# Performance work log

Hardware: AMD Instinct MI355X
Metric: run time of the kernel (lower is better)

Reference implementation:

```python
import jax, jax.numpy as jnp
import numpy as np

NEG_SLOPE = 0.01  # torch F.leaky_relu default


def _leaky_relu(v):
    return jnp.where(v >= 0, v, NEG_SLOPE * v)


def _att_layer(t, w1, w2):
    # t: [b, c, n] ; SE-style channel attention with scalar gate
    y = t.mean(axis=-1)                                   # [b, c] (AdaptiveAvgPool1d(1))
    y = jax.nn.sigmoid(jax.nn.relu(y @ w1.T) @ w2.T)       # [b, 1]
    return t * y[:, :, None]


def _avwgcn(x, node_emb, supports, cheb, wpool, bpool, iw, ib, gw, gb,
            a1w1, a1w2, a2w1, a2w2):
    # x: [b, n, c_in]; supports/cheb: [k, n, n]
    b, n, _ = x.shape
    weights = jnp.einsum('nd,dkio->nkio', node_emb, wpool)   # per-node dyn weights
    bias = node_emb @ bpool                                  # [n, o]
    x_g = jnp.einsum('knm,bmc->bnkc', supports, x)           # [b, n, k, c_in]
    x_gconv0 = jnp.einsum('bnki,nkio->bno', x_g, weights) + bias
    x0 = x @ iw.T + ib                                       # init_gconv: [b, n, o]
    x_g1 = jnp.einsum('knm,bmc->bnkc', cheb, x0).reshape(b, n, -1)
    x_gconv1 = x_g1 @ gw.T + gb                              # [b, n, o]
    out = (_att_layer(_leaky_relu(x_gconv0).transpose(0, 2, 1), a1w1, a1w2)
           + _att_layer(_leaky_relu(x_gconv1).transpose(0, 2, 1), a2w1, a2w2))
    return out.transpose(0, 2, 1)                            # [b, n, o]


def _cheb_supports(L, k):
    n = L.shape[0]
    s = [jnp.eye(n, dtype=L.dtype), L]
    for _ in range(2, k):
        s.append(2.0 * L @ s[-1] - s[-2])
    return jnp.stack(s, axis=0)  # [k, n, n]


B, N, DIN, DOUT, K, ED = 64, 1024, 32, 64, 3, 16
CIN = DIN + DOUT  # 96 (gate/update input = cat(x, state))


def setup_inputs() -> dict:
    key = jax.random.key(0)
    ks = jax.random.split(key, 32)
    g = lambda i, shape, s=0.1: jax.random.normal(ks[i], shape, dtype=jnp.float32) * s
    inp = {
        'x': jax.random.normal(ks[0], (B, N, DIN), dtype=jnp.float32),
        'state': jax.random.normal(ks[1], (B, N, DOUT), dtype=jnp.float32),
        'node_embeddings': jax.random.normal(ks[2], (N, ED), dtype=jnp.float32),
        'learned_tilde': jax.random.normal(ks[3], (N, N), dtype=jnp.float32) / np.sqrt(N),
        'cheb_polynomials': jax.random.normal(ks[4], (K, N, N), dtype=jnp.float32) / np.sqrt(N),
        # gate AVWGCN: dim_in=96, dim_out=2*DOUT=128
        'gate_wpool': g(5, (ED, K, CIN, 2 * DOUT)),
        'gate_bpool': g(6, (ED, 2 * DOUT)),
        'gate_iw': g(7, (2 * DOUT, CIN)), 'gate_ib': g(8, (2 * DOUT,)),
        'gate_gw': g(9, (2 * DOUT, 2 * DOUT * K)), 'gate_gb': g(10, (2 * DOUT,)),
        'gate_a1w1': g(11, (2 * DOUT // 16, 2 * DOUT)), 'gate_a1w2': g(12, (1, 2 * DOUT // 16)),
        'gate_a2w1': g(13, (2 * DOUT // 16, 2 * DOUT)), 'gate_a2w2': g(14, (1, 2 * DOUT // 16)),
        # update AVWGCN: dim_in=96, dim_out=DOUT=64
        'upd_wpool': g(15, (ED, K, CIN, DOUT)),
        'upd_bpool': g(16, (ED, DOUT)),
        'upd_iw': g(17, (DOUT, CIN)), 'upd_ib': g(18, (DOUT,)),
        'upd_gw': g(19, (DOUT, DOUT * K)), 'upd_gb': g(20, (DOUT,)),
        'upd_a1w1': g(21, (DOUT // 16, DOUT)), 'upd_a1w2': g(22, (1, DOUT // 16)),
        'upd_a2w1': g(23, (DOUT // 16, DOUT)), 'upd_a2w2': g(24, (1, DOUT // 16)),
    }
    return inp


def reference(x, state, node_embeddings, learned_tilde, cheb_polynomials,
              gate_wpool, gate_bpool, gate_iw, gate_ib, gate_gw, gate_gb,
              gate_a1w1, gate_a1w2, gate_a2w1, gate_a2w2,
              upd_wpool, upd_bpool, upd_iw, upd_ib, upd_gw, upd_gb,
              upd_a1w1, upd_a1w2, upd_a2w1, upd_a2w2):
    supports = _cheb_supports(learned_tilde, K)  # [k, n, n]
    inp_state = jnp.concatenate([x, state], axis=-1)  # [b, n, din+dout]
    z_r = jax.nn.sigmoid(_avwgcn(inp_state, node_embeddings, supports, cheb_polynomials,
                                 gate_wpool, gate_bpool, gate_iw, gate_ib, gate_gw, gate_gb,
                                 gate_a1w1, gate_a1w2, gate_a2w1, gate_a2w2))
    z, r = jnp.split(z_r, 2, axis=-1)
    candidate = jnp.concatenate([x, z * state], axis=-1)
    hc = jnp.tanh(_avwgcn(candidate, node_embeddings, supports, cheb_polynomials,
                          upd_wpool, upd_bpool, upd_iw, upd_ib, upd_gw, upd_gb,
                          upd_a1w1, upd_a1w2, upd_a2w1, upd_a2w2))
    h = r * state + (1.0 - r) * hc
    return h
```

## Files before the change

### kernel.cpp

```cpp
#include <hip/hip_runtime.h>
#include <hip/hip_bf16.h>
#include <math.h>


#define B_  64
#define N_  1024
#define CIN_ 96
#define R_  288

typedef __attribute__((ext_vector_type(8))) short bf16x8;
typedef __attribute__((ext_vector_type(4))) float f32x4;
typedef unsigned short u16;
typedef unsigned int u32;

__device__ __forceinline__ float lrelu(float v) { return v >= 0.f ? v : 0.01f * v; }
__device__ __forceinline__ float sigmoidf_(float u) { return 1.f / (1.f + expf(-u)); }
__device__ __forceinline__ u16 f2b(float f) {
  union { float f; u32 u; } c; c.f = f;
  u32 u = c.u;
  return (u16)((u + 0x7FFFu + ((u >> 16) & 1u)) >> 16);
}
__device__ __forceinline__ float b2f(u16 u) {
  union { u32 x; float f; } c; c.x = ((u32)u) << 16; return c.f;
}
__device__ __forceinline__ void gload_lds16(const u16* gp, u16* lp) {
  __builtin_amdgcn_global_load_lds((const __attribute__((address_space(1))) u32*)gp,
                                   (__attribute__((address_space(3))) u32*)lp, 16, 0, 0);
}

__global__ __launch_bounds__(256) void concat_bf2(const float* __restrict__ x,
                                                  const float* __restrict__ st,
                                                  float* __restrict__ inp,
                                                  u16* __restrict__ inpb) {
  size_t t = (size_t)blockIdx.x * 256 + threadIdx.x;
  if (t >= (size_t)B_ * N_ * CIN_) return;
  int i = (int)(t % CIN_);
  size_t v = t / CIN_;
  size_t b = v & 63, n = v >> 6;
  float f = (i < 32) ? x[(b * N_ + n) * 32 + i] : st[(b * N_ + n) * 64 + (i - 32)];
  inp[t] = f;
  inpb[t] = f2b(f);
}

__global__ __launch_bounds__(256) void conv_f2b(const float* __restrict__ in,
                                                u16* __restrict__ out, int n4) {
  int t = blockIdx.x * 256 + threadIdx.x;
  if (t >= n4) return;
  float4 v = ((const float4*)in)[t];
  ushort4 o;
  o.x = f2b(v.x); o.y = f2b(v.y); o.z = f2b(v.z); o.w = f2b(v.w);
  ((ushort4*)out)[t] = o;
}

__global__ __launch_bounds__(256) void split_hilo(const float* __restrict__ in,
                                                  u16* __restrict__ hi,
                                                  u16* __restrict__ lo, int n4) {
  int t = blockIdx.x * 256 + threadIdx.x;
  if (t >= n4) return;
  float4 v = ((const float4*)in)[t];
  ushort4 h, l;
  h.x = f2b(v.x); l.x = f2b(v.x - b2f(h.x));
  h.y = f2b(v.y); l.y = f2b(v.y - b2f(h.y));
  h.z = f2b(v.z); l.z = f2b(v.z - b2f(h.z));
  h.w = f2b(v.w); l.w = f2b(v.w - b2f(h.w));
  ((ushort4*)hi)[t] = h;
  ((ushort4*)lo)[t] = l;
}

__global__ __launch_bounds__(256) void transpose_split(const float* __restrict__ in,
                                                       u16* __restrict__ hiT,
                                                       u16* __restrict__ loT) {
  __shared__ float t[32][33];
  const int tid = threadIdx.x;
  const int j0 = blockIdx.x * 32, r0 = blockIdx.y * 32;
  const int tc = tid & 31, tr = tid >> 5;
#pragma unroll
  for (int q = 0; q < 4; ++q)
    t[tr + q * 8][tc] = in[(size_t)(r0 + tr + q * 8) * 1024 + j0 + tc];
  __syncthreads();
  const int jj = tid >> 3, rq = (tid & 7) * 4;
  ushort4 h, l;
#pragma unroll
  for (int q = 0; q < 4; ++q) {
    float v = t[rq + q][jj];
    u16 hh = f2b(v);
    ((u16*)&h)[q] = hh;
    ((u16*)&l)[q] = f2b(v - b2f(hh));
  }
  *(ushort4*)(hiT + (size_t)(j0 + jj) * N_ + r0 + rq) = h;
  *(ushort4*)(loT + (size_t)(j0 + jj) * N_ + r0 + rq) = l;
}

__global__ __launch_bounds__(256) void transpose_b2b(const u16* __restrict__ Z, int Zs,
                                                     int Ctot, u16* __restrict__ Zt) {
  __shared__ u16 t[32][36];
  const int tid = threadIdx.x;
  const int c0 = blockIdx.x * 32, n0 = blockIdx.y * 32, b = blockIdx.z;
  {
    const int i = tid >> 3, c4 = (tid & 7) * 4;
    ushort4 v = *(const ushort4*)(Z + ((size_t)(n0 + i) * 64 + b) * Zs + c0 + c4);
    t[i][c4] = v.x; t[i][c4 + 1] = v.y; t[i][c4 + 2] = v.z; t[i][c4 + 3] = v.w;
  }
  __syncthreads();
  {
    const int c = tid >> 3, n4 = (tid & 7) * 4;
    ushort4 o;
    o.x = t[n4][c]; o.y = t[n4 + 1][c]; o.z = t[n4 + 2][c]; o.w = t[n4 + 3][c];
    *(ushort4*)(Zt + (size_t)(b * Ctot + c0 + c) * 1024 + n0 + n4) = o;
  }
}

__global__ __launch_bounds__(256) void mfma_l2p(const u16* __restrict__ Lhi,
                                                const u16* __restrict__ Llo,
                                                const u16* __restrict__ LhiT,
                                                const u16* __restrict__ LloT,
                                                float* __restrict__ P) {
  __shared__ u16 Asl[64 * 64];
  __shared__ u16 Bsl[64 * 64];
  const int tid = threadIdx.x;
  const int w = tid >> 6, lane = tid & 63;
  const int m0 = blockIdx.y * 64, n0 = blockIdx.x * 64;
  const int ph = blockIdx.z;
  const int wr = w >> 1, wc = w & 1;
  const int sr = lane >> 3, so = lane & 7;
  const int cl = lane & 15, q4 = lane >> 4;
  f32x4 acc[2][2] = {};

  const u16* A = (ph == 1) ? Llo : Lhi;
  const u16* B = (ph == 2) ? LloT : LhiT;
  for (int k0 = 0; k0 < 1024; k0 += 64) {
    __syncthreads();
#pragma unroll
    for (int i = 0; i < 2; ++i) {
      const int r = i * 32 + w * 8 + sr;
      const int o = so ^ (r & 7);
      gload_lds16(A + (size_t)(m0 + r) * 1024 + k0 + o * 8, Asl + (i * 32 + w * 8) * 64);
      gload_lds16(B + (size_t)(n0 + r) * 1024 + k0 + o * 8, Bsl + (i * 32 + w * 8) * 64);
    }
    __syncthreads();
#pragma unroll
    for (int kk = 0; kk < 2; ++kk) {
      bf16x8 af[2], bfr[2];
#pragma unroll
      for (int mi = 0; mi < 2; ++mi) {
        const int ra = wr * 32 + mi * 16 + cl;
        af[mi] = *(const bf16x8*)(Asl + ra * 64 + ((kk * 4 + q4) ^ (ra & 7)) * 8);
      }
#pragma unroll
      for (int ni = 0; ni < 2; ++ni) {
        const int rb = wc * 32 + ni * 16 + cl;
        bfr[ni] = *(const bf16x8*)(Bsl + rb * 64 + ((kk * 4 + q4) ^ (rb & 7)) * 8);
      }
#pragma unroll
      for (int mi = 0; mi < 2; ++mi)
#pragma unroll
        for (int ni = 0; ni < 2; ++ni)
          acc[mi][ni] = __builtin_amdgcn_mfma_f32_16x16x32_bf16(af[mi], bfr[ni], acc[mi][ni], 0, 0, 0);
    }
  }
  float* Pz = P + ((size_t)ph << 20);
#pragma unroll
  for (int mi = 0; mi < 2; ++mi)
#pragma unroll
    for (int ni = 0; ni < 2; ++ni) {
      const int j = n0 + wc * 32 + ni * 16 + cl;
#pragma unroll
      for (int r = 0; r < 4; ++r) {
        const int m = m0 + wr * 32 + mi * 16 + q4 * 4 + r;
        Pz[(size_t)m * 1024 + j] = acc[mi][ni][r];
      }
    }
}

__global__ __launch_bounds__(256) void l2_finish(const float* __restrict__ P,
                                                 u16* __restrict__ Y) {
  int t = blockIdx.x * 256 + threadIdx.x;
  float4 a = ((const float4*)P)[t];
  float4 b = ((const float4*)(P + 1048576))[t];
  float4 c = ((const float4*)(P + 2097152))[t];
  int e = t << 2;
  int m = e >> 10, j = e & 1023;
  ushort4 o;
  o.x = f2b(2.f * (a.x + b.x + c.x) - (m == j     ? 1.f : 0.f));
  o.y = f2b(2.f * (a.y + b.y + c.y) - (m == j + 1 ? 1.f : 0.f));
  o.z = f2b(2.f * (a.z + b.z + c.z) - (m == j + 2 ? 1.f : 0.f));
  o.w = f2b(2.f * (a.w + b.w + c.w) - (m == j + 3 ? 1.f : 0.f));
  ((ushort4*)Y)[t] = o;
}

__global__ __launch_bounds__(512) void mfma_stack_w(const u16* __restrict__ A,
                                                    const u16* __restrict__ Bt,
                                                    float* __restrict__ Y, int J) {
  __shared__ u16 Asl[2][128 * 64];
  __shared__ u16 Bsl[2][256 * 64];
  const int tid = threadIdx.x;
  const int w = tid >> 6, lane = tid & 63;
  const int m0 = blockIdx.y * 128, n0 = blockIdx.x * 256;
  const int wr = w >> 2, wc = w & 3;
  const int sr = lane >> 3, so = lane & 7;
  const int cl = lane & 15, q4 = lane >> 4;
  f32x4 acc[4][4] = {};

  auto STAGE = [&](u16* Ad, u16* Bd, int k0) {
#pragma unroll
    for (int i = 0; i < 2; ++i) {
      const int r = i * 64 + w * 8 + sr;
      const int o = so ^ (r & 7);
      gload_lds16(A + (size_t)(m0 + r) * 1024 + k0 + o * 8, Ad + (i * 64 + w * 8) * 64);
    }
#pragma unroll
    for (int i = 0; i < 4; ++i) {
      const int r = i * 64 + w * 8 + sr;
      const int o = so ^ (r & 7);
      gload_lds16(Bt + (size_t)(n0 + r) * 1024 + k0 + o * 8, Bd + (i * 64 + w * 8) * 64);
    }
  };
  auto COMPUTE = [&](const u16* As, const u16* Bs) {
#pragma unroll
    for (int kk = 0; kk < 2; ++kk) {
      bf16x8 af[4], bfr[4];
#pragma unroll
      for (int mi = 0; mi < 4; ++mi) {
        const int ra = wr * 64 + mi * 16 + cl;
        af[mi] = *(const bf16x8*)(As + ra * 64 + ((kk * 4 + q4) ^ (ra & 7)) * 8);
      }
#pragma unroll
      for (int ni = 0; ni < 4; ++ni) {
        const int rb = wc * 64 + ni * 16 + cl;
        bfr[ni] = *(const bf16x8*)(Bs + rb * 64 + ((kk * 4 + q4) ^ (rb & 7)) * 8);
      }
#pragma unroll
      for (int mi = 0; mi < 4; ++mi)
#pragma unroll
        for (int ni = 0; ni < 4; ++ni)
          acc[mi][ni] = __builtin_amdgcn_mfma_f32_16x16x32_bf16(af[mi], bfr[ni], acc[mi][ni], 0, 0, 0);
    }
  };

  STAGE(Asl[0], Bsl[0], 0);
  for (int k0 = 0; k0 < 1024; k0 += 128) {
    STAGE(Asl[1], Bsl[1], k0 + 64);
    asm volatile("s_waitcnt vmcnt(6)" ::: "memory");
    __builtin_amdgcn_s_barrier();
    __builtin_amdgcn_sched_barrier(0);
    COMPUTE(Asl[0], Bsl[0]);
    asm volatile("s_waitcnt lgkmcnt(0)" ::: "memory");
    __builtin_amdgcn_s_barrier();
    __builtin_amdgcn_sched_barrier(0);
    if (k0 + 128 < 1024) {
      STAGE(Asl[0], Bsl[0], k0 + 128);
      asm volatile("s_waitcnt vmcnt(6)" ::: "memory");
    } else {
      asm volatile("s_waitcnt vmcnt(0)" ::: "memory");
    }
    __builtin_amdgcn_s_barrier();
    __builtin_amdgcn_sched_barrier(0);
    COMPUTE(Asl[1], Bsl[1]);
    asm volatile("s_waitcnt lgkmcnt(0)" ::: "memory");
    __builtin_amdgcn_s_barrier();
    __builtin_amdgcn_sched_barrier(0);
  }
#pragma unroll
  for (int mi = 0; mi < 4; ++mi)
#pragma unroll
    for (int ni = 0; ni < 4; ++ni) {
      const int j = n0 + wc * 64 + ni * 16 + cl;
#pragma unroll
      for (int r = 0; r < 4; ++r) {
        const int m = m0 + wr * 64 + mi * 16 + q4 * 4 + r;
        Y[(size_t)m * J + j] = acc[mi][ni][r];
      }
    }
}

template <int O, int OSH>
__global__ __launch_bounds__(128) void vgen2(const float* __restrict__ gw,
                                             const float* __restrict__ iw,
                                             const float* __restrict__ ib,
                                             int Ctot,
                                             u16* __restrict__ Vb,
                                             float* __restrict__ ball) {
  const int c = blockIdx.x;
  const int col = threadIdx.x;
  if (c >= Ctot) {
    if (col < 96) Vb[(size_t)c * 96 + col] = 0;
    else if (col == 96) ball[c] = 0.f;
    return;
  }
  __shared__ float sg[O];
  const int o = c & (O - 1), k = c >> OSH;
  const float* g = gw + (size_t)o * (3 * O) + (size_t)k * O;
  for (int e = col; e < O; e += 128) sg[e] = g[e];
  __syncthreads();
  if (col < 96) {
    float s = 0.f;
#pragma unroll
    for (int j = 0; j < O; ++j) s += sg[j] * iw[j * 96 + col];
    Vb[(size_t)c * 96 + col] = f2b(s);
  } else if (col == 96) {
    float s = 0.f;
#pragma unroll
    for (int j = 0; j < O; ++j) s += sg[j] * ib[j];
    ball[c] = s;
  }
}

__global__ __launch_bounds__(256) void zgemm(const u16* __restrict__ A,
                                             const u16* __restrict__ Bt,
                                             const float* __restrict__ ball,
                                             u16* __restrict__ Z, int Zs) {
  __shared__ u16 Asl[128 * 32];
  __shared__ u16 Bsl[128 * 32];
  const int tid = threadIdx.x;
  const int w = tid >> 6, lane = tid & 63;
  const int m0 = blockIdx.y * 128, n0 = blockIdx.x * 128;
  const int wr = w >> 1, wc = w & 1;
  const int sr = lane >> 2, so = lane & 3;
  const int cl = lane & 15, q4 = lane >> 4;
  f32x4 acc[4][4] = {};
  for (int k0 = 0; k0 < 96; k0 += 32) {
    __syncthreads();
#pragma unroll
    for (int i = 0; i < 2; ++i) {
      const int r = i * 64 + w * 16 + sr;
      const int o = so ^ (r & 3);
      gload_lds16(A + (size_t)(m0 + r) * 96 + k0 + o * 8, Asl + (i * 64 + w * 16) * 32);
      gload_lds16(Bt + (size_t)(n0 + r) * 96 + k0 + o * 8, Bsl + (i * 64 + w * 16) * 32);
    }
    __syncthreads();
    bf16x8 af[4], bfr[4];
#pragma unroll
    for (int mi = 0; mi < 4; ++mi) {
      const int ra = wr * 64 + mi * 16 + cl;
      af[mi] = *(const bf16x8*)(Asl + ra * 32 + (q4 ^ (ra & 3)) * 8);
    }
#pragma unroll
    for (int ni = 0; ni < 4; ++ni) {
      const int rb = wc * 64 + ni * 16 + cl;
      bfr[ni] = *(const bf16x8*)(Bsl + rb * 32 + (q4 ^ (rb & 3)) * 8);
    }
#pragma unroll
    for (int mi = 0; mi < 4; ++mi)
#pragma unroll
      for (int ni = 0; ni < 4; ++ni)
        acc[mi][ni] = __builtin_amdgcn_mfma_f32_16x16x32_bf16(af[mi], bfr[ni], acc[mi][ni], 0, 0, 0);
  }
#pragma unroll
  for (int mi = 0; mi < 4; ++mi)
#pragma unroll
    for (int ni = 0; ni < 4; ++ni) {
      const int c = n0 + wc * 64 + ni * 16 + cl;
      const float bb = ball[c];
#pragma unroll
      for (int r = 0; r < 4; ++r) {
        const int m = m0 + wr * 64 + mi * 16 + q4 * 4 + r;
        Z[(size_t)m * Zs + c] = f2b(acc[mi][ni][r] + bb);
      }
    }
}

__global__ __launch_bounds__(512) void mfma_k3(const u16* __restrict__ A3,
                                               const u16* __restrict__ Zt,
                                               const float* __restrict__ gb,
                                               float* __restrict__ Y,
                                               int J, int obits) {
  __shared__ u16 Asl[2][128 * 64];
  __shared__ u16 Bsl[2][128 * 64];
  const int tid = threadIdx.x;
  const int w = tid >> 6, lane = tid & 63;
  const int m0 = blockIdx.y * 128, n0 = blockIdx.x * 128;
  const int wr = w >> 2, wc = w & 3;
  const int sr = lane >> 3, so = lane & 7;
  const int cl = lane & 15, q4 = lane >> 4;
  const int omask = (1 << obits) - 1;
  f32x4 acc[4][2] = {};

  auto STAGE = [&](u16* Ad, u16* Bd, int k0) {
    const int kb = k0 >> 10, ko = k0 & 1023;
#pragma unroll
    for (int i = 0; i < 2; ++i) {
      const int r = i * 64 + w * 8 + sr;
      const int o = so ^ (r & 7);
      gload_lds16(A3 + (size_t)kb * 1048576 + (size_t)(m0 + r) * 1024 + ko + o * 8,
                  Ad + (i * 64 + w * 8) * 64);
      const int jp = n0 + r;
      const int brow = (((jp >> obits) * 3 + kb) << obits) | (jp & omask);
      gload_lds16(Zt + (size_t)brow * 1024 + ko + o * 8, Bd + (i * 64 + w * 8) * 64);
    }
  };
  auto COMPUTE = [&](const u16* As, const u16* Bs) {
#pragma unroll
    for (int kk = 0; kk < 2; ++kk) {
      bf16x8 af[4], bfr[2];
#pragma unroll
      for (int mi = 0; mi < 4; ++mi) {
        const int ra = wr * 64 + mi * 16 + cl;
        af[mi] = *(const bf16x8*)(As + ra * 64 + ((kk * 4 + q4) ^ (ra & 7)) * 8);
      }
#pragma unroll
      for (int ni = 0; ni < 2; ++ni) {
        const int rb = wc * 32 + ni * 16 + cl;
        bfr[ni] = *(const bf16x8*)(Bs + rb * 64 + ((kk * 4 + q4) ^ (rb & 7)) * 8);
      }
#pragma unroll
      for (int mi = 0; mi < 4; ++mi)
#pragma unroll
        for (int ni = 0; ni < 2; ++ni)
          acc[mi][ni] = __builtin_amdgcn_mfma_f32_16x16x32_bf16(af[mi], bfr[ni], acc[mi][ni], 0, 0, 0);
    }
  };

  STAGE(Asl[0], Bsl[0], 0);
  for (int k0 = 0; k0 < 3072; k0 += 128) {
    STAGE(Asl[1], Bsl[1], k0 + 64);
    asm volatile("s_waitcnt vmcnt(4)" ::: "memory");
    __builtin_amdgcn_s_barrier();
    __builtin_amdgcn_sched_barrier(0);
    COMPUTE(Asl[0], Bsl[0]);
    asm volatile("s_waitcnt lgkmcnt(0)" ::: "memory");
    __builtin_amdgcn_s_barrier();
    __builtin_amdgcn_sched_barrier(0);
    if (k0 + 128 < 3072) {
      STAGE(Asl[0], Bsl[0], k0 + 128);
      asm volatile("s_waitcnt vmcnt(4)" ::: "memory");
    } else {
      asm volatile("s_waitcnt vmcnt(0)" ::: "memory");
    }
    __builtin_amdgcn_s_barrier();
    __builtin_amdgcn_sched_barrier(0);
    COMPUTE(Asl[1], Bsl[1]);
    asm volatile("s_waitcnt lgkmcnt(0)" ::: "memory");
    __builtin_amdgcn_s_barrier();
    __builtin_amdgcn_sched_barrier(0);
  }
#pragma unroll
  for (int mi = 0; mi < 4; ++mi)
#pragma unroll
    for (int ni = 0; ni < 2; ++ni) {
      const int j = n0 + wc * 32 + ni * 16 + cl;
      const float bb = gb[j & omask];
#pragma unroll
      for (int r = 0; r < 4; ++r) {
        const int m = m0 + wr * 64 + mi * 16 + q4 * 4 + r;
        Y[(size_t)m * J + j] = acc[mi][ni][r] + bb;
      }
    }
}

__global__ __launch_bounds__(512) void mfma_k3w(const u16* __restrict__ A3,
                                                const u16* __restrict__ Zt,
                                                const float* __restrict__ gb,
                                                float* __restrict__ Y,
                                                int J, int obits) {
  __shared__ u16 Asl[2][128 * 64];
  __shared__ u16 Bsl[2][256 * 64];
  const int tid = threadIdx.x;
  const int w = tid >> 6, lane = tid & 63;
  const int m0 = blockIdx.y * 128, n0 = blockIdx.x * 256;
  const int wr = w >> 2, wc = w & 3;
  const int sr = lane >> 3, so = lane & 7;
  const int cl = lane & 15, q4 = lane >> 4;
  const int omask = (1 << obits) - 1;
  f32x4 acc[4][4] = {};

  auto STAGE = [&](u16* Ad, u16* Bd, int k0) {
    const int kb = k0 >> 10, ko = k0 & 1023;
#pragma unroll
    for (int i = 0; i < 2; ++i) {
      const int r = i * 64 + w * 8 + sr;
      const int o = so ^ (r & 7);
      gload_lds16(A3 + (size_t)kb * 1048576 + (size_t)(m0 + r) * 1024 + ko + o * 8,
                  Ad + (i * 64 + w * 8) * 64);
    }
#pragma unroll
    for (int i = 0; i < 4; ++i) {
      const int r = i * 64 + w * 8 + sr;
      const int o = so ^ (r & 7);
      const int jp = n0 + r;
      const int brow = (((jp >> obits) * 3 + kb) << obits) | (jp & omask);
      gload_lds16(Zt + (size_t)brow * 1024 + ko + o * 8, Bd + (i * 64 + w * 8) * 64);
    }
  };
  auto COMPUTE = [&](const u16* As, const u16* Bs) {
#pragma unroll
    for (int kk = 0; kk < 2; ++kk) {
      bf16x8 af[4], bfr[4];
#pragma unroll
      for (int mi = 0; mi < 4; ++mi) {
        const int ra = wr * 64 + mi * 16 + cl;
        af[mi] = *(const bf16x8*)(As + ra * 64 + ((kk * 4 + q4) ^ (ra & 7)) * 8);
      }
#pragma unroll
      for (int ni = 0; ni < 4; ++ni) {
        const int rb = wc * 64 + ni * 16 + cl;
        bfr[ni] = *(const bf16x8*)(Bs + rb * 64 + ((kk * 4 + q4) ^ (rb & 7)) * 8);
      }
#pragma unroll
      for (int mi = 0; mi < 4; ++mi)
#pragma unroll
        for (int ni = 0; ni < 4; ++ni)
          acc[mi][ni] = __builtin_amdgcn_mfma_f32_16x16x32_bf16(af[mi], bfr[ni], acc[mi][ni], 0, 0, 0);
    }
  };

  STAGE(Asl[0], Bsl[0], 0);
  for (int k0 = 0; k0 < 3072; k0 += 128) {
    STAGE(Asl[1], Bsl[1], k0 + 64);
    asm volatile("s_waitcnt vmcnt(6)" ::: "memory");
    __builtin_amdgcn_s_barrier();
    __builtin_amdgcn_sched_barrier(0);
    COMPUTE(Asl[0], Bsl[0]);
    asm volatile("s_waitcnt lgkmcnt(0)" ::: "memory");
    __builtin_amdgcn_s_barrier();
    __builtin_amdgcn_sched_barrier(0);
    if (k0 + 128 < 3072) {
      STAGE(Asl[0], Bsl[0], k0 + 128);
      asm volatile("s_waitcnt vmcnt(6)" ::: "memory");
    } else {
      asm volatile("s_waitcnt vmcnt(0)" ::: "memory");
    }
    __builtin_amdgcn_s_barrier();
    __builtin_amdgcn_sched_barrier(0);
    COMPUTE(Asl[1], Bsl[1]);
    asm volatile("s_waitcnt lgkmcnt(0)" ::: "memory");
    __builtin_amdgcn_s_barrier();
    __builtin_amdgcn_sched_barrier(0);
  }
#pragma unroll
  for (int mi = 0; mi < 4; ++mi)
#pragma unroll
    for (int ni = 0; ni < 4; ++ni) {
      const int j = n0 + wc * 64 + ni * 16 + cl;
      const float bb = gb[j & omask];
#pragma unroll
      for (int r = 0; r < 4; ++r) {
        const int m = m0 + wr * 64 + mi * 16 + q4 * 4 + r;
        Y[(size_t)m * J + j] = acc[mi][ni][r] + bb;
      }
    }
}

template <int OW>
__global__ __launch_bounds__(256) void weightgen3w(const float* __restrict__ emb,
                                                   const float* __restrict__ wpool,
                                                   u16* __restrict__ W) {
  const int tid = threadIdx.x;
  const int ro = blockIdx.x * 256 + tid;
  const int r = ro / OW, o = ro % OW;
  const int n0 = blockIdx.y * 64;
  __shared__ float semb[64][17];
  for (int e = tid; e < 1024; e += 256) semb[e >> 4][e & 15] = emb[(n0 + (e >> 4)) * 16 + (e & 15)];
  __syncthreads();
  float wv[16];
#pragma unroll
  for (int d = 0; d < 16; ++d) wv[d] = wpool[((size_t)d * R_ + r) * OW + o];
#pragma unroll 4
  for (int n = 0; n < 64; ++n) {
    float s = 0.f;
#pragma unroll
    for (int d = 0; d < 16; ++d) s += semb[n][d] * wv[d];
    W[(size_t)(n0 + n) * (R_ * OW) + ro] = f2b(s);
  }
}

template <int OW>
__global__ __launch_bounds__(256) void pernode9(const float* __restrict__ xa,
                                                const float* __restrict__ xbc,
                                                const u16* __restrict__ W,
                                                const float* __restrict__ emb,
                                                const float* __restrict__ bpool,
                                                float* __restrict__ outp) {
  constexpr int QO = OW / 32;
  const int n = blockIdx.x;
  const int tid = threadIdx.x;
  __shared__ __align__(16) float sW[32][OW + 4];
  __shared__ __align__(16) float sX[32][68];
  __shared__ float semb[16];
  if (tid < 16) semb[tid] = emb[n * 16 + tid];
  const int tx = tid & 31, tb = tid >> 5;
  const int lb = tid >> 2, li = (tid & 3) * 8;
  float acc[8][QO] = {};
  const u16* Wn = W + (size_t)n * (R_ * OW);

  for (int c = 0; c < 9; ++c) {
    const int k = c / 3, i0 = (c % 3) * 32;
    const float* xk = (k == 0) ? (xa + (size_t)n * 6144)
                               : (xbc + ((size_t)(k - 1) * 1024 + n) * 6144);
    __syncthreads();
    {
#pragma unroll
      for (int it = 0; it < OW / 64; ++it) {
        const int slot = it * 256 + tid;
        const int row = slot / (OW / 8), o8 = (slot % (OW / 8)) * 8;
        uint4 v = *(const uint4*)(Wn + (size_t)(c * 32 + row) * OW + o8);
        float4 f0, f1;
        f0.x = b2f((u16)(v.x & 0xFFFF)); f0.y = b2f((u16)(v.x >> 16));
        f0.z = b2f((u16)(v.y & 0xFFFF)); f0.w = b2f((u16)(v.y >> 16));
        f1.x = b2f((u16)(v.z & 0xFFFF)); f1.y = b2f((u16)(v.z >> 16));
        f1.z = b2f((u16)(v.w & 0xFFFF)); f1.w = b2f((u16)(v.w >> 16));
        *(float4*)&sW[row][o8] = f0;
        *(float4*)&sW[row][o8 + 4] = f1;
      }
    }
    {
      const float* p = xk + (size_t)lb * 96 + i0 + li;
      float4 v0 = *(const float4*)p;
      float4 v1 = *(const float4*)(p + 4);
      sX[li + 0][lb] = v0.x; sX[li + 1][lb] = v0.y;
      sX[li + 2][lb] = v0.z; sX[li + 3][lb] = v0.w;
      sX[li + 4][lb] = v1.x; sX[li + 5][lb] = v1.y;
      sX[li + 6][lb] = v1.z; sX[li + 7][lb] = v1.w;
    }
    __syncthreads();
#pragma unroll
    for (int il = 0; il < 32; ++il) {
      float4 xv0 = *(const float4*)&sX[il][tb * 8];
      float4 xv1 = *(const float4*)&sX[il][tb * 8 + 4];
      float xv[8] = {xv0.x, xv0.y, xv0.z, xv0.w, xv1.x, xv1.y, xv1.z, xv1.w};
      float wv[QO];
      if constexpr (QO == 4) {
        float4 w4 = *(const float4*)&sW[il][tx * 4];
        wv[0] = w4.x; wv[1] = w4.y; wv[2] = w4.z; wv[3] = w4.w;
      } else {
        float2 w2 = *(const float2*)&sW[il][tx * 2];
        wv[0] = w2.x; wv[1] = w2.y;
      }
#pragma unroll
      for (int j = 0; j < 8; ++j)
#pragma unroll
        for (int q = 0; q < QO; ++q) acc[j][q] += xv[j] * wv[q];
    }
  }
  float bias[QO];
#pragma unroll
  for (int q = 0; q < QO; ++q) {
    int o = tx * QO + q;
    float s = 0.f;
#pragma unroll
    for (int d = 0; d < 16; ++d) s += semb[d] * bpool[d * OW + o];
    bias[q] = s;
  }
#pragma unroll
  for (int j = 0; j < 8; ++j) {
    size_t base = ((size_t)n * B_ + tb * 8 + j) * OW + tx * QO;
#pragma unroll
    for (int q = 0; q < QO; ++q) outp[base + q] = acc[j][q] + bias[q];
  }
}

template <int C>
__global__ __launch_bounds__(256) void att_reduce(const float* __restrict__ A0,
                                                  const float* __restrict__ A1,
                                                  float* __restrict__ part0,
                                                  float* __restrict__ part1) {
  constexpr int C4 = C / 4;
  constexpr int H = 256 / C4;
  const int chunk = blockIdx.x;
  const int b = blockIdx.y;
  const int tid = threadIdx.x;
  const int c4 = tid % C4, h = tid / C4;
  __shared__ float4 r0[256], r1[256];
  float4 s0 = {0.f, 0.f, 0.f, 0.f}, s1 = {0.f, 0.f, 0.f, 0.f};
  const float4* p0 = (const float4*)(A0 + (size_t)b * C) + c4;
  const float4* p1 = (const float4*)(A1 + (size_t)b * C) + c4;
  const size_t stride = (size_t)B_ * C4;
  for (int n = chunk * 64 + h; n < chunk * 64 + 64; n += H) {
    float4 v0 = p0[(size_t)n * stride];
    float4 v1 = p1[(size_t)n * stride];
    s0.x += lrelu(v0.x); s0.y += lrelu(v0.y); s0.z += lrelu(v0.z); s0.w += lrelu(v0.w);
    s1.x += lrelu(v1.x); s1.y += lrelu(v1.y); s1.z += lrelu(v1.z); s1.w += lrelu(v1.w);
  }
  r0[tid] = s0; r1[tid] = s1;
  __syncthreads();
  if (h == 0) {
    for (int hh = 1; hh < H; ++hh) {
      float4 a = r0[c4 + hh * C4], bb = r1[c4 + hh * C4];
      s0.x += a.x; s0.y += a.y; s0.z += a.z; s0.w += a.w;
      s1.x += bb.x; s1.y += bb.y; s1.z += bb.z; s1.w += bb.w;
    }
    ((float4*)(part0 + ((size_t)b * 16 + chunk) * C))[c4] = s0;
    ((float4*)(part1 + ((size_t)b * 16 + chunk) * C))[c4] = s1;
  }
}

template <int C, int HID>
__global__ __launch_bounds__(256) void att_finish(const float* __restrict__ part0,
                                                  const float* __restrict__ part1,
                                                  const float* __restrict__ w11,
                                                  const float* __restrict__ w12,
                                                  const float* __restrict__ w21,
                                                  const float* __restrict__ w22,
                                                  float* __restrict__ sout) {
  const int b = blockIdx.x;
  const int tid = threadIdx.x;
  __shared__ float sm0[C], sm1[C];
  __shared__ float h0[HID], h1[HID];
  if (tid < C) {
    float s0 = 0.f, s1 = 0.f;
    for (int ch = 0; ch < 16; ++ch) {
      s0 += part0[((size_t)b * 16 + ch) * C + tid];
      s1 += part1[((size_t)b * 16 + ch) * C + tid];
    }
    sm0[tid] = s0 * (1.f / N_); sm1[tid] = s1 * (1.f / N_);
  }
  __syncthreads();
  if (tid < HID) {
    float a = 0.f;
    for (int cc = 0; cc < C; ++cc) a += sm0[cc] * w11[tid * C + cc];
    h0[tid] = fmaxf(a, 0.f);
  } else if (tid >= 32 && tid < 32 + HID) {
    int j = tid - 32;
    float a = 0.f;
    for (int cc = 0; cc < C; ++cc) a += sm1[cc] * w21[j * C + cc];
    h1[j] = fmaxf(a, 0.f);
  }
  __syncthreads();
  if (tid == 0) {
    float a = 0.f;
    for (int j = 0; j < HID; ++j) a += h0[j] * w12[j];
    sout[b] = sigmoidf_(a);
  } else if (tid == 32) {
    float a = 0.f;
    for (int j = 0; j < HID; ++j) a += h1[j] * w22[j];
    sout[B_ + b] = sigmoidf_(a);
  }
}

__global__ __launch_bounds__(256) void gate_combine_b2(const float* __restrict__ a0,
                                                       const float* __restrict__ a1,
                                                       const float* __restrict__ s12,
                                                       const float* __restrict__ x,
                                                       const float* __restrict__ st,
                                                       float* __restrict__ cand,
                                                       u16* __restrict__ candb,
                                                       float* __restrict__ rbuf) {
  size_t t = (size_t)blockIdx.x * 256 + threadIdx.x;
  if (t >= (size_t)B_ * N_ * 64) return;
  int c = (int)(t & 63);
  int b = (int)((t >> 6) & 63);
  int n = (int)(t >> 12);
  float s1 = s12[b], s2 = s12[B_ + b];
  size_t nb = (size_t)n * B_ + b;
  size_t i128 = nb * 128;
  float uz = s1 * lrelu(a0[i128 + c]) + s2 * lrelu(a1[i128 + c]);
  float ur = s1 * lrelu(a0[i128 + 64 + c]) + s2 * lrelu(a1[i128 + 64 + c]);
  float z = sigmoidf_(uz);
  float r = sigmoidf_(ur);
  float stv = st[((size_t)b * N_ + n) * 64 + c];
  float zs = z * stv;
  cand[nb * CIN_ + 32 + c] = zs;
  candb[nb * CIN_ + 32 + c] = f2b(zs);
  rbuf[nb * 64 + c] = r;
  if (c < 32) {
    float xv = x[((size_t)b * N_ + n) * 32 + c];
    cand[nb * CIN_ + c] = xv;
    candb[nb * CIN_ + c] = f2b(xv);
  }
}

__global__ __launch_bounds__(256) void final_h(const float* __restrict__ a0,
                                               const float* __restrict__ a1,
                                               const float* __restrict__ s12,
                                               const float* __restrict__ rbuf,
                                               const float* __restrict__ st,
                                               float* __restrict__ out) {
  size_t t = (size_t)blockIdx.x * 256 + threadIdx.x;
  if (t >= (size_t)B_ * N_ * 64) return;
  int o = (int)(t & 63);
  int n = (int)((t >> 6) & 1023);
  int b = (int)(t >> 16);
  float s1 = s12[b], s2 = s12[B_ + b];
  size_t nb = ((size_t)n * B_ + b) * 64 + o;
  float u = s1 * lrelu(a0[nb]) + s2 * lrelu(a1[nb]);
  float hc = tanhf(u);
  float r = rbuf[nb];
  out[t] = r * st[t] + (1.f - r) * hc;
}

extern "C" void kernel_launch(void* const* d_in, const int* in_sizes, int n_in,
                              void* d_out, int out_size, void* d_ws, size_t ws_size,
                              hipStream_t stream) {
  const float* x       = (const float*)d_in[0];
  const float* state   = (const float*)d_in[1];
  const float* emb     = (const float*)d_in[2];
  const float* Ltil    = (const float*)d_in[3];
  const float* cheb    = (const float*)d_in[4];
  const float* g_wpool = (const float*)d_in[5];
  const float* g_bpool = (const float*)d_in[6];
  const float* g_iw    = (const float*)d_in[7];
  const float* g_ib    = (const float*)d_in[8];
  const float* g_gw    = (const float*)d_in[9];
  const float* g_gb    = (const float*)d_in[10];
  const float* g_a1w1  = (const float*)d_in[11];
  const float* g_a1w2  = (const float*)d_in[12];
  const float* g_a2w1  = (const float*)d_in[13];
  const float* g_a2w2  = (const float*)d_in[14];
  const float* u_wpool = (const float*)d_in[15];
  const float* u_bpool = (const float*)d_in[16];
  const float* u_iw    = (const float*)d_in[17];
  const float* u_ib    = (const float*)d_in[18];
  const float* u_gw    = (const float*)d_in[19];
  const float* u_gb    = (const float*)d_in[20];
  const float* u_a1w1  = (const float*)d_in[21];
  const float* u_a1w2  = (const float*)d_in[22];
  const float* u_a2w1  = (const float*)d_in[23];
  const float* u_a2w2  = (const float*)d_in[24];
  float* out = (float*)d_out;

  float* ws    = (float*)d_ws;
  float* inp   = ws;
  u16*   inpb  = (u16*)(ws + 6291456);
  float* t12   = ws + 9437184;
  u16*   Zbuf  = (u16*)t12;
  u16*   Wbuf  = (u16*)(ws + 22020096);
  u16*   Wbuf128 = Wbuf;
  u16*   Btp   = (u16*)(ws + 31457280);
  u16*   Zt    = Wbuf;
  float* acc1  = ws + 34603008;
  float* acc0  = ws + 42991616;
  u16*   LbStk = (u16*)(ws + 51380224);
  u16*   chebb = (u16*)(ws + 52428800);
  float* s12   = ws + 54001664;
  float* s12u  = ws + 54001792;
  float* part0 = ws + 54001920;
  float* part1 = ws + 54132992;
  float* rbuf  = ws + 54264064;
  u16*   Vbg   = (u16*)(ws + 58458368);
  float* bag   = ws + 58476800;
  u16*   Vbu   = (u16*)(ws + 58477184);
  float* bau   = ws + 58489472;
  u16*   LhiT  = (u16*)(ws + 58489728);
  u16*   LloT  = (u16*)(ws + 59014016);
  u16*   Llo   = (u16*)(ws + 59538304);

  dim3 blk(256);
  dim3 blk512(512);

  split_hilo<<<1024, blk, 0, stream>>>(Ltil, LbStk, Llo, 262144);
  transpose_split<<<dim3(32, 32), blk, 0, stream>>>(Ltil, LhiT, LloT);
  mfma_l2p<<<dim3(16, 16, 3), blk, 0, stream>>>(LbStk, Llo, LhiT, LloT, t12);
  l2_finish<<<1024, blk, 0, stream>>>(t12, LbStk + 1048576);
  conv_f2b<<<3072, blk, 0, stream>>>(cheb, chebb, 786432);

  concat_bf2<<<24576, blk, 0, stream>>>(x, state, inp, inpb);
  transpose_b2b<<<dim3(3, 32, 64), blk, 0, stream>>>(inpb, 96, 96, Btp);
  mfma_stack_w<<<dim3(24, 16), blk512, 0, stream>>>(LbStk, Btp, t12, 6144);
  vgen2<128, 7><<<384, dim3(128), 0, stream>>>(g_gw, g_iw, g_ib, 384, Vbg, bag);
  weightgen3w<128><<<dim3(144, 16), blk, 0, stream>>>(emb, g_wpool, Wbuf128);
  pernode9<128><<<1024, blk, 0, stream>>>(inp, t12, Wbuf128, emb, g_bpool, acc0);
  zgemm<<<dim3(3, 512), blk, 0, stream>>>(inpb, Vbg, bag, Zbuf, 384);
  transpose_b2b<<<dim3(12, 32, 64), blk, 0, stream>>>(Zbuf, 384, 384, Zt);
  mfma_k3w<<<dim3(32, 8), blk512, 0, stream>>>(chebb, Zt, g_gb, acc1, 8192, 7);
  att_reduce<128><<<dim3(16, 64), blk, 0, stream>>>(acc0, acc1, part0, part1);
  att_finish<128, 8><<<64, blk, 0, stream>>>(part0, part1, g_a1w1, g_a1w2, g_a2w1, g_a2w2, s12);
  gate_combine_b2<<<16384, blk, 0, stream>>>(acc0, acc1, s12, x, state, inp, inpb, rbuf);

  transpose_b2b<<<dim3(3, 32, 64), blk, 0, stream>>>(inpb, 96, 96, Btp);
  mfma_stack_w<<<dim3(24, 16), blk512, 0, stream>>>(LbStk, Btp, t12, 6144);
  vgen2<64, 6><<<256, dim3(128), 0, stream>>>(u_gw, u_iw, u_ib, 192, Vbu, bau);
  weightgen3w<64><<<dim3(72, 16), blk, 0, stream>>>(emb, u_wpool, Wbuf);
  pernode9<64><<<1024, blk, 0, stream>>>(inp, t12, Wbuf, emb, u_bpool, acc0);
  zgemm<<<dim3(2, 512), blk, 0, stream>>>(inpb, Vbu, bau, Zbuf, 256);
  transpose_b2b<<<dim3(6, 32, 64), blk, 0, stream>>>(Zbuf, 256, 192, Zt);
  mfma_k3<<<dim3(32, 8), blk512, 0, stream>>>(chebb, Zt, u_gb, acc1, 4096, 6);
  att_reduce<64><<<dim3(16, 64), blk, 0, stream>>>(acc0, acc1, part0, part1);
  att_finish<64, 4><<<64, blk, 0, stream>>>(part0, part1, u_a1w1, u_a1w2, u_a2w1, u_a2w2, s12u);
  final_h<<<16384, blk, 0, stream>>>(acc0, acc1, s12u, rbuf, state, out);
}
```

Before: 695.8 us.

## Move per-node dynamic-weight GEMM to bf16 MFMA with hi/lo split inputs

Rewrites the per-node graph-conv kernel so it uses bf16 MFMA 16x16x32 instructions instead of scalar fp32 FMAs. Activations are split into bf16 hi and lo parts to keep accuracy, which doubles the MFMA count. To feed the A operand, wpool is now transposed up front and the generated per-node weights are stored output-major. Weights go global-to-LDS directly with XOR swizzles, which removes the bf16-to-fp32 unpack in shared memory. The cost is two extra small transpose launches and the reuse of workspace regions that earlier kernels had already consumed.

Result: faster. 631.2 us (-9.3%).

```diff
diff --git a/kernel.cpp b/kernel.cpp
--- a/kernel.cpp
+++ b/kernel.cpp
@@ -108,6 +108,22 @@
     o.x = t[n4][c]; o.y = t[n4 + 1][c]; o.z = t[n4 + 2][c]; o.w = t[n4 + 3][c];
     *(ushort4*)(Zt + (size_t)(b * Ctot + c0 + c) * 1024 + n0 + n4) = o;
   }
+}
+
+__global__ __launch_bounds__(256) void wpool_tr(const float* __restrict__ wp,
+                                                float* __restrict__ wpT, int OW) {
+  __shared__ float t[32][33];
+  const int tid = threadIdx.x;
+  const int r0 = blockIdx.x * 32, o0 = blockIdx.y * 32, d = blockIdx.z;
+  const size_t base = (size_t)d * 288 * OW;
+  const int c = tid & 31, q0 = tid >> 5;
+#pragma unroll
+  for (int q = 0; q < 4; ++q)
+    t[q0 + q * 8][c] = wp[base + (size_t)(r0 + q0 + q * 8) * OW + o0 + c];
+  __syncthreads();
+#pragma unroll
+  for (int q = 0; q < 4; ++q)
+    wpT[base + (size_t)(o0 + q0 + q * 8) * 288 + r0 + c] = t[c][q0 + q * 8];
 }
 
 __global__ __launch_bounds__(256) void mfma_l2p(const u16* __restrict__ Lhi,
@@ -540,112 +556,125 @@
     }
 }
 
-template <int OW>
-__global__ __launch_bounds__(256) void weightgen3w(const float* __restrict__ emb,
-                                                   const float* __restrict__ wpool,
-                                                   u16* __restrict__ W) {
+template <int SZ>
+__global__ __launch_bounds__(256) void weightgen5(const float* __restrict__ emb,
+                                                  const float* __restrict__ wpT,
+                                                  u16* __restrict__ W) {
   const int tid = threadIdx.x;
   const int ro = blockIdx.x * 256 + tid;
-  const int r = ro / OW, o = ro % OW;
   const int n0 = blockIdx.y * 64;
   __shared__ float semb[64][17];
   for (int e = tid; e < 1024; e += 256) semb[e >> 4][e & 15] = emb[(n0 + (e >> 4)) * 16 + (e & 15)];
   __syncthreads();
   float wv[16];
 #pragma unroll
-  for (int d = 0; d < 16; ++d) wv[d] = wpool[((size_t)d * R_ + r) * OW + o];
+  for (int d = 0; d < 16; ++d) wv[d] = wpT[(size_t)d * SZ + ro];
 #pragma unroll 4
   for (int n = 0; n < 64; ++n) {
     float s = 0.f;
 #pragma unroll
     for (int d = 0; d < 16; ++d) s += semb[n][d] * wv[d];
-    W[(size_t)(n0 + n) * (R_ * OW) + ro] = f2b(s);
+    W[(size_t)(n0 + n) * SZ + ro] = f2b(s);
   }
 }
 
 template <int OW>
-__global__ __launch_bounds__(256) void pernode9(const float* __restrict__ xa,
-                                                const float* __restrict__ xbc,
-                                                const u16* __restrict__ W,
-                                                const float* __restrict__ emb,
-                                                const float* __restrict__ bpool,
-                                                float* __restrict__ outp) {
-  constexpr int QO = OW / 32;
+__global__ __launch_bounds__(256) void pernode10(const float* __restrict__ xa,
+                                                 const float* __restrict__ xbc,
+                                                 const u16* __restrict__ Wt,
+                                                 const float* __restrict__ emb,
+                                                 const float* __restrict__ bpool,
+                                                 float* __restrict__ outp) {
+  constexpr int MT = OW / 64;
   const int n = blockIdx.x;
   const int tid = threadIdx.x;
-  __shared__ __align__(16) float sW[32][OW + 4];
-  __shared__ __align__(16) float sX[32][68];
+  const int w = tid >> 6, lane = tid & 63;
+  const int cl = lane & 15, q4 = lane >> 4;
+  __shared__ u16 sWt[OW * 32];
+  __shared__ u16 sXh[64 * 32];
+  __shared__ u16 sXl[64 * 32];
   __shared__ float semb[16];
   if (tid < 16) semb[tid] = emb[n * 16 + tid];
-  const int tx = tid & 31, tb = tid >> 5;
-  const int lb = tid >> 2, li = (tid & 3) * 8;
-  float acc[8][QO] = {};
-  const u16* Wn = W + (size_t)n * (R_ * OW);
+  f32x4 acc[MT][4] = {};
+  const u16* Wn = Wt + (size_t)n * (OW * 288);
+  const int xb = tid >> 2, rg = tid & 3;
 
   for (int c = 0; c < 9; ++c) {
     const int k = c / 3, i0 = (c % 3) * 32;
     const float* xk = (k == 0) ? (xa + (size_t)n * 6144)
                                : (xbc + ((size_t)(k - 1) * 1024 + n) * 6144);
     __syncthreads();
+#pragma unroll
+    for (int i = 0; i < MT; ++i) {
+      const int g = w * MT + i;
+      const int o = g * 16 + (lane >> 2);
+      const int seg = (lane & 3) ^ (o & 3);
+      gload_lds16(Wn + (size_t)o * 288 + c * 32 + seg * 8, sWt + g * 512);
+    }
     {
-#pragma unroll
-      for (int it = 0; it < OW / 64; ++it) {
-        const int slot = it * 256 + tid;
-        const int row = slot / (OW / 8), o8 = (slot % (OW / 8)) * 8;
-        uint4 v = *(const uint4*)(Wn + (size_t)(c * 32 + row) * OW + o8);
-        float4 f0, f1;
-        f0.x = b2f((u16)(v.x & 0xFFFF)); f0.y = b2f((u16)(v.x >> 16));
-        f0.z = b2f((u16)(v.y & 0xFFFF)); f0.w = b2f((u16)(v.y >> 16));
-        f1.x = b2f((u16)(v.z & 0xFFFF)); f1.y = b2f((u16)(v.z >> 16));
-        f1.z = b2f((u16)(v.w & 0xFFFF)); f1.w = b2f((u16)(v.w >> 16));
-        *(float4*)&sW[row][o8] = f0;
-        *(float4*)&sW[row][o8 + 4] = f1;
-      }
-    }
-    {
-      const float* p = xk + (size_t)lb * 96 + i0 + li;
+      const float* p = xk + (size_t)xb * 96 + i0 + rg * 8;
       float4 v0 = *(const float4*)p;
       float4 v1 = *(const float4*)(p + 4);
-      sX[li + 0][lb] = v0.x; sX[li + 1][lb] = v0.y;
-      sX[li + 2][lb] = v0.z; sX[li + 3][lb] = v0.w;
-      sX[li + 4][lb] = v1.x; sX[li + 5][lb] = v1.y;
-      sX[li + 6][lb] = v1.z; sX[li + 7][lb] = v1.w;
+      float xv[8] = {v0.x, v0.y, v0.z, v0.w, v1.x, v1.y, v1.z, v1.w};
+      bf16x8 h, l;
+#pragma unroll
+      for (int j = 0; j < 8; ++j) {
+        u16 hh = f2b(xv[j]);
+        ((u16*)&h)[j] = hh;
+        ((u16*)&l)[j] = f2b(xv[j] - b2f(hh));
+      }
+      const int col = (rg ^ (xb & 3)) * 8;
+      *(bf16x8*)(sXh + xb * 32 + col) = h;
+      *(bf16x8*)(sXl + xb * 32 + col) = l;
     }
     __syncthreads();
-#pragma unroll
-    for (int il = 0; il < 32; ++il) {
-      float4 xv0 = *(const float4*)&sX[il][tb * 8];
-      float4 xv1 = *(const float4*)&sX[il][tb * 8 + 4];
-      float xv[8] = {xv0.x, xv0.y, xv0.z, xv0.w, xv1.x, xv1.y, xv1.z, xv1.w};
-      float wv[QO];
-      if constexpr (QO == 4) {
-        float4 w4 = *(const float4*)&sW[il][tx * 4];
-        wv[0] = w4.x; wv[1] = w4.y; wv[2] = w4.z; wv[3] = w4.w;
-      } else {
-        float2 w2 = *(const float2*)&sW[il][tx * 2];
-        wv[0] = w2.x; wv[1] = w2.y;
-      }
-#pragma unroll
-      for (int j = 0; j < 8; ++j)
-#pragma unroll
-        for (int q = 0; q < QO; ++q) acc[j][q] += xv[j] * wv[q];
-    }
-  }
-  float bias[QO];
-#pragma unroll
-  for (int q = 0; q < QO; ++q) {
-    int o = tx * QO + q;
-    float s = 0.f;
-#pragma unroll
-    for (int d = 0; d < 16; ++d) s += semb[d] * bpool[d * OW + o];
-    bias[q] = s;
-  }
-#pragma unroll
-  for (int j = 0; j < 8; ++j) {
-    size_t base = ((size_t)n * B_ + tb * 8 + j) * OW + tx * QO;
-#pragma unroll
-    for (int q = 0; q < QO; ++q) outp[base + q] = acc[j][q] + bias[q];
-  }
+    bf16x8 aw[MT], bh[4], bl[4];
+#pragma unroll
+    for (int mi = 0; mi < MT; ++mi) {
+      const int o = (w * MT + mi) * 16 + cl;
+      aw[mi] = *(const bf16x8*)(sWt + o * 32 + ((q4 ^ (o & 3)) * 8));
+    }
+#pragma unroll
+    for (int ni = 0; ni < 4; ++ni) {
+      const int b = ni * 16 + cl;
+      const int col = (q4 ^ (b & 3)) * 8;
+      bh[ni] = *(const bf16x8*)(sXh + b * 32 + col);
+      bl[ni] = *(const bf16x8*)(sXl + b * 32 + col);
+    }
+#pragma unroll
+    for (int mi = 0; mi < MT; ++mi)
+#pragma unroll
+      for (int ni = 0; ni < 4; ++ni)
+        acc[mi][ni] = __builtin_amdgcn_mfma_f32_16x16x32_bf16(aw[mi], bh[ni], acc[mi][ni], 0, 0, 0);
+#pragma unroll
+    for (int mi = 0; mi < MT; ++mi)
+#pragma unroll
+      for (int ni = 0; ni < 4; ++ni)
+        acc[mi][ni] = __builtin_amdgcn_mfma_f32_16x16x32_bf16(aw[mi], bl[ni], acc[mi][ni], 0, 0, 0);
+  }
+  float4 biasv[MT];
+#pragma unroll
+  for (int mi = 0; mi < MT; ++mi)
+#pragma unroll
+    for (int r = 0; r < 4; ++r) {
+      const int o = (w * MT + mi) * 16 + q4 * 4 + r;
+      float s = 0.f;
+#pragma unroll
+      for (int d = 0; d < 16; ++d) s += semb[d] * bpool[d * OW + o];
+      ((float*)&biasv[mi])[r] = s;
+    }
+#pragma unroll
+  for (int mi = 0; mi < MT; ++mi)
+#pragma unroll
+    for (int ni = 0; ni < 4; ++ni) {
+      const int b = ni * 16 + cl;
+      float4 v;
+      v.x = acc[mi][ni][0] + biasv[mi].x;
+      v.y = acc[mi][ni][1] + biasv[mi].y;
+      v.z = acc[mi][ni][2] + biasv[mi].z;
+      v.w = acc[mi][ni][3] + biasv[mi].w;
+      *(float4*)(outp + ((size_t)n * 64 + b) * OW + (w * MT + mi) * 16 + q4 * 4) = v;
+    }
 }
 
 template <int C>
@@ -832,6 +861,8 @@
   u16*   LhiT  = (u16*)(ws + 58489728);
   u16*   LloT  = (u16*)(ws + 59014016);
   u16*   Llo   = (u16*)(ws + 59538304);
+  float* wpTg  = ws + 58489728;
+  float* wpTu  = ws + 59079552;
 
   dim3 blk(256);
   dim3 blk512(512);
@@ -839,6 +870,8 @@
   split_hilo<<<1024, blk, 0, stream>>>(Ltil, LbStk, Llo, 262144);
   transpose_split<<<dim3(32, 32), blk, 0, stream>>>(Ltil, LhiT, LloT);
   mfma_l2p<<<dim3(16, 16, 3), blk, 0, stream>>>(LbStk, Llo, LhiT, LloT, t12);
+  wpool_tr<<<dim3(9, 4, 16), blk, 0, stream>>>(g_wpool, wpTg, 128);
+  wpool_tr<<<dim3(9, 2, 16), blk, 0, stream>>>(u_wpool, wpTu, 64);
   l2_finish<<<1024, blk, 0, stream>>>(t12, LbStk + 1048576);
   conv_f2b<<<3072, blk, 0, stream>>>(cheb, chebb, 786432);
 
@@ -846,8 +879,8 @@
   transpose_b2b<<<dim3(3, 32, 64), blk, 0, stream>>>(inpb, 96, 96, Btp);
   mfma_stack_w<<<dim3(24, 16), blk512, 0, stream>>>(LbStk, Btp, t12, 6144);
   vgen2<128, 7><<<384, dim3(128), 0, stream>>>(g_gw, g_iw, g_ib, 384, Vbg, bag);
-  weightgen3w<128><<<dim3(144, 16), blk, 0, stream>>>(emb, g_wpool, Wbuf128);
-  pernode9<128><<<1024, blk, 0, stream>>>(inp, t12, Wbuf128, emb, g_bpool, acc0);
+  weightgen5<36864><<<dim3(144, 16), blk, 0, stream>>>(emb, wpTg, Wbuf128);
+  pernode10<128><<<1024, blk, 0, stream>>>(inp, t12, Wbuf128, emb, g_bpool, acc0);
   zgemm<<<dim3(3, 512), blk, 0, stream>>>(inpb, Vbg, bag, Zbuf, 384);
   transpose_b2b<<<dim3(12, 32, 64), blk, 0, stream>>>(Zbuf, 384, 384, Zt);
   mfma_k3w<<<dim3(32, 8), blk512, 0, stream>>>(chebb, Zt, g_gb, acc1, 8192, 7);
@@ -858,8 +891,8 @@
   transpose_b2b<<<dim3(3, 32, 64), blk, 0, stream>>>(inpb, 96, 96, Btp);
   mfma_stack_w<<<dim3(24, 16), blk512, 0, stream>>>(LbStk, Btp, t12, 6144);
   vgen2<64, 6><<<256, dim3(128), 0, stream>>>(u_gw, u_iw, u_ib, 192, Vbu, bau);
-  weightgen3w<64><<<dim3(72, 16), blk, 0, stream>>>(emb, u_wpool, Wbuf);
-  pernode9<64><<<1024, blk, 0, stream>>>(inp, t12, Wbuf, emb, u_bpool, acc0);
+  weightgen5<18432><<<dim3(72, 16), blk, 0, stream>>>(emb, wpTu, Wbuf);
+  pernode10<64><<<1024, blk, 0, stream>>>(inp, t12, Wbuf, emb, u_bpool, acc0);
   zgemm<<<dim3(2, 512), blk, 0, stream>>>(inpb, Vbu, bau, Zbuf, 256);
   transpose_b2b<<<dim3(6, 32, 64), blk, 0, stream>>>(Zbuf, 256, 192, Zt);
   mfma_k3<<<dim3(32, 8), blk512, 0, stream>>>(chebb, Zt, u_gb, acc1, 4096, 6);
```
